# Kernel optimization log

Measured on AMD Instinct MI355X. Metric: run time of the kernel, lower is better.

The kernel has to match this reference:

```python
import jax, jax.numpy as jnp
import numpy as np

DIM = 64
K = 8
B_TAIL = 3.0
HID = 128
BATCH = 131072
MIN_BIN_WIDTH = 1e-3
MIN_BIN_HEIGHT = 1e-3
MIN_DERIVATIVE = 1e-3


def setup_inputs() -> dict:
    key = jax.random.key(0)
    ks = jax.random.split(key, 9)
    nin = DIM // 2
    nout = (3 * K - 1) * (DIM - DIM // 2)
    dims = [nin, HID, HID, HID, nout]
    d = {"x": jax.random.normal(ks[0], (BATCH, DIM), jnp.float32)}
    for i in range(4):
        d[f"W{i+1}"] = jax.random.normal(ks[1 + 2 * i], (dims[i], dims[i + 1]), jnp.float32) / jnp.sqrt(dims[i])
        d[f"b{i+1}"] = jax.random.normal(ks[2 + 2 * i], (dims[i + 1],), jnp.float32) * 0.01
    return d


def _gather(a, idx):
    # a: [..., K or K+1], idx: [...] int -> [...]
    return jnp.take_along_axis(a, idx[..., None], axis=-1)[..., 0]


def _mlp(x, W1, b1, W2, b2, W3, b3, W4, b4):
    h = jax.nn.elu(x @ W1 + b1)
    h = jax.nn.elu(h @ W2 + b2)
    h = jax.nn.elu(h @ W3 + b3)
    return h @ W4 + b4


def _unconstrained_rqs_fwd(inputs, uw, uh, ud, tail_bound):
    # inputs: [B, D2]; uw/uh: [B, D2, K]; ud: [B, D2, K-1]
    num_bins = uw.shape[-1]
    left = bottom = -tail_bound
    right = top = tail_bound

    inside = (inputs >= -tail_bound) & (inputs <= tail_bound)
    x = jnp.clip(inputs, -tail_bound, tail_bound)  # safe values for spline math

    # pad derivatives and pin boundary slopes so spline matches identity tails
    const = float(np.log(np.exp(1.0 - MIN_DERIVATIVE) - 1.0))
    ud = jnp.pad(ud, [(0, 0)] * (ud.ndim - 1) + [(1, 1)], constant_values=const)

    widths = jax.nn.softmax(uw, axis=-1)
    widths = MIN_BIN_WIDTH + (1.0 - MIN_BIN_WIDTH * num_bins) * widths
    cumwidths = jnp.cumsum(widths, axis=-1)
    cumwidths = jnp.pad(cumwidths, [(0, 0)] * (cumwidths.ndim - 1) + [(1, 0)])
    cumwidths = (right - left) * cumwidths + left
    cumwidths = cumwidths.at[..., 0].set(left).at[..., -1].set(right)
    widths = cumwidths[..., 1:] - cumwidths[..., :-1]

    derivatives = MIN_DERIVATIVE + jax.nn.softplus(ud)

    heights = jax.nn.softmax(uh, axis=-1)
    heights = MIN_BIN_HEIGHT + (1.0 - MIN_BIN_HEIGHT * num_bins) * heights
    cumheights = jnp.cumsum(heights, axis=-1)
    cumheights = jnp.pad(cumheights, [(0, 0)] * (cumheights.ndim - 1) + [(1, 0)])
    cumheights = (top - bottom) * cumheights + bottom
    cumheights = cumheights.at[..., 0].set(bottom).at[..., -1].set(top)
    heights = cumheights[..., 1:] - cumheights[..., :-1]

    # searchsorted: number of bin edges <= x, minus one (eps on last edge)
    cw = cumwidths.at[..., -1].add(1e-6)
    bin_idx = jnp.sum((x[..., None] >= cw).astype(jnp.int32), axis=-1) - 1
    bin_idx = jnp.clip(bin_idx, 0, num_bins - 1)

    in_cw = _gather(cumwidths, bin_idx)
    in_w = _gather(widths, bin_idx)
    in_ch = _gather(cumheights, bin_idx)
    in_h = _gather(heights, bin_idx)
    delta = heights / widths
    in_delta = _gather(delta, bin_idx)
    in_d = _gather(derivatives, bin_idx)
    in_d1 = _gather(derivatives[..., 1:], bin_idx)

    theta = (x - in_cw) / in_w
    t1mt = theta * (1.0 - theta)
    numerator = in_h * (in_delta * theta ** 2 + in_d * t1mt)
    denominator = in_delta + (in_d + in_d1 - 2.0 * in_delta) * t1mt
    spline_out = in_ch + numerator / denominator
    deriv_num = in_delta ** 2 * (in_d1 * theta ** 2 + 2.0 * in_delta * t1mt + in_d * (1.0 - theta) ** 2)
    spline_ld = jnp.log(deriv_num) - 2.0 * jnp.log(denominator)

    outputs = jnp.where(inside, spline_out, inputs)
    logabsdet = jnp.where(inside, spline_ld, 0.0)
    return outputs, logabsdet


def reference(x, W1, b1, W2, b2, W3, b3, W4, b4):
    d_half = DIM // 2
    x1, x2 = x[:, :d_half], x[:, d_half:]
    out = _mlp(x1, W1, b1, W2, b2, W3, b3, W4, b4)
    out = out.reshape(-1, DIM - d_half, 3 * K - 1)
    W = out[..., :K]
    H = out[..., K:2 * K]
    D = out[..., 2 * K:]
    y2, ld = _unconstrained_rqs_fwd(x2, W, H, D, B_TAIL)
    log_det = jnp.sum(ld, axis=1)
    return jnp.concatenate([x1, y2], axis=1), log_det
```

## Files before the change

### kernel.cpp

```cpp
#include <hip/hip_runtime.h>
#include <hip/hip_bf16.h>
#include <math.h>

typedef _Float16 f16_t;
typedef _Float16 f16x4 __attribute__((ext_vector_type(4)));
typedef _Float16 f16x8 __attribute__((ext_vector_type(8)));
typedef float f32x4 __attribute__((ext_vector_type(4)));

#define BATCH 131072
#define MTILE 64
#define NBLK (BATCH / MTILE)
#define LOG2E 1.4426950408889634f

#define W1F 0
#define W2F 4096
#define W3F 20480
#define W4F 36864
#define B4S_OFF 67584

__global__ __launch_bounds__(256) void convert_weights_kernel(
    const float* __restrict__ W1, const float* __restrict__ W2,
    const float* __restrict__ W3, const float* __restrict__ W4,
    const float* __restrict__ b4, f16_t* __restrict__ wf,
    float* __restrict__ b4s) {
  int tid = blockIdx.x * 256 + threadIdx.x;
  if (tid >= 16896) {
    int i = tid - 16896;
    if (i < 736) {
      float s = ((i % 23) < 16) ? LOG2E : 1.f;
      b4s[i] = b4[i] * s;
    }
    return;
  }
  int lane = tid & 63;
  int l16 = lane & 15, lhi = lane >> 4;
  const float* W; int ncols, col, k0; bool zero = false; float scale = 1.f;
  if (tid < 512) {
    int n = tid >> 6;
    W = W1; ncols = 128; col = n * 16 + l16; k0 = lhi * 8;
  } else if (tid < 2560) {
    int g = tid - 512; int n = g >> 8, s = (g >> 6) & 3;
    W = W2; ncols = 128; col = n * 16 + l16; k0 = s * 32 + lhi * 8;
  } else if (tid < 4608) {
    int g = tid - 2560; int n = g >> 8, s = (g >> 6) & 3;
    W = W3; ncols = 128; col = n * 16 + l16; k0 = s * 32 + lhi * 8;
  } else {
    int g = tid - 4608; int t = g >> 8, s = (g >> 6) & 3;
    int c = t / 6, n = t - c * 6;
    int colc = n * 16 + l16;
    W = W4; ncols = 736; col = c * 92 + colc; k0 = s * 32 + lhi * 8;
    zero = (colc >= 92);
    if (!zero) scale = ((col % 23) < 16) ? LOG2E : 1.f;
  }
  f16x8 v;
#pragma unroll
  for (int j = 0; j < 8; ++j)
    v[j] = zero ? (f16_t)0.f : (f16_t)(W[(k0 + j) * ncols + col] * scale);
  *(f16x8*)(wf + (size_t)tid * 8) = v;
}

__device__ __forceinline__ float elu(float v) {
  return v > 0.f ? v : (__expf(v) - 1.f);
}

__device__ __forceinline__ void rqs_task(const f16_t* P, float xv,
                                         float& yout, float& ldout) {
  f16x8 pw = *(const f16x8*)P;
  f16x8 ph = *(const f16x8*)(P + 8);
  f16x8 pd = *(const f16x8*)(P + 16);

  float ew[8], sw = 0.f;
#pragma unroll
  for (int i = 0; i < 8; ++i) { ew[i] = exp2f((float)pw[i]); sw += ew[i]; }
  float invw = 0.992f * __builtin_amdgcn_rcpf(sw);
  float cw[8]; cw[0] = -3.f;
  float accw = 0.f;
#pragma unroll
  for (int i = 0; i < 7; ++i) {
    accw += 0.001f + ew[i] * invw;
    cw[i + 1] = -3.f + 6.f * accw;
  }

  float eh[8], sh = 0.f;
#pragma unroll
  for (int i = 0; i < 8; ++i) { eh[i] = exp2f((float)ph[i]); sh += eh[i]; }
  float invh = 0.992f * __builtin_amdgcn_rcpf(sh);
  float ch[8]; ch[0] = -3.f;
  float acch = 0.f;
#pragma unroll
  for (int i = 0; i < 7; ++i) {
    acch += 0.001f + eh[i] * invh;
    ch[i + 1] = -3.f + 6.f * acch;
  }

  float xc = fminf(fmaxf(xv, -3.f), 3.f);
  int bin = 0;
#pragma unroll
  for (int i = 1; i < 8; ++i) bin += (xc >= cw[i]) ? 1 : 0;

  float in_cw = cw[0], in_ch = ch[0];
  float ewsel = ew[0], ehsel = eh[0];
  float sd  = (float)pd[0];
  float sd1 = (float)pd[0];
#pragma unroll
  for (int i = 1; i < 8; ++i) {
    bool g = (bin >= i);
    in_cw = g ? cw[i] : in_cw;  in_ch = g ? ch[i] : in_ch;
    ewsel = g ? ew[i] : ewsel;  ehsel = g ? eh[i] : ehsel;
    sd    = g ? (float)pd[i - 1] : sd;
  }
#pragma unroll
  for (int i = 1; i < 7; ++i)
    sd1 = (bin >= i) ? (float)pd[i] : sd1;

  float in_w = fmaf(ewsel * invw, 6.f, 0.006f);
  float in_h = fmaf(ehsel * invh, 6.f, 0.006f);

  float spd  = fmaxf(sd,  0.f) + __logf(1.f + __expf(-fabsf(sd)));
  float spd1 = fmaxf(sd1, 0.f) + __logf(1.f + __expf(-fabsf(sd1)));
  float in_d  = (bin == 0) ? 1.f : 0.001f + spd;
  float in_d1 = (bin == 7) ? 1.f : 0.001f + spd1;

  float rw = __builtin_amdgcn_rcpf(in_w);
  float dlt = in_h * rw;
  float th = (xc - in_cw) * rw;
  float om = 1.f - th;
  float t1 = th * om;
  float num = in_h * (dlt * th * th + in_d * t1);
  float den = dlt + (in_d + in_d1 - 2.f * dlt) * t1;
  float rden = __builtin_amdgcn_rcpf(den);
  float yo = in_ch + num * rden;
  float dn = dlt * dlt * (in_d1 * th * th + 2.f * dlt * t1 + in_d * om * om);
  float ldv = __logf(dn * rden * rden);
  bool inside = (xv >= -3.f) && (xv <= 3.f);
  yout = inside ? yo : xv;
  ldout = inside ? ldv : 0.f;
}

__device__ __forceinline__ void mid_layer_ip(f16_t* hH,
                                             const f16_t* __restrict__ wseg,
                                             const float* __restrict__ bg,
                                             int wv, int l16, int lhi, int lane) {
  f16x8 a[4];
#pragma unroll
  for (int s = 0; s < 4; ++s)
    a[s] = *(const f16x8*)&hH[(wv * 16 + l16) * 136 + s * 32 + lhi * 8];
#pragma unroll
  for (int n = 0; n < 8; ++n) {
    f32x4 acc = {0.f, 0.f, 0.f, 0.f};
#pragma unroll
    for (int s = 0; s < 4; ++s) {
      f16x8 b = *(const f16x8*)(wseg + (size_t)((n * 4 + s) * 64 + lane) * 8);
      acc = __builtin_amdgcn_mfma_f32_16x16x32_f16(a[s], b, acc, 0, 0, 0);
    }
    float bias = bg[n * 16 + l16];
#pragma unroll
    for (int r = 0; r < 4; ++r)
      hH[(wv * 16 + lhi * 4 + r) * 136 + n * 16 + l16] =
          (f16_t)elu(acc[r] + bias);
  }
}

__global__ __launch_bounds__(256, 3) void nsf_fused_kernel(
    const float* __restrict__ x,
    const float* __restrict__ b1g, const float* __restrict__ b2g,
    const float* __restrict__ b3g, const float* __restrict__ b4s,
    const f16_t* __restrict__ wf,
    float* __restrict__ out) {
  __shared__ f16_t hH[MTILE * 136];
  __shared__ float x2s[MTILE * 33];

  const int tid = threadIdx.x;
  const int lane = tid & 63;
  const int wv = tid >> 6;
  const int l16 = lane & 15, lhi = lane >> 4;
  const int row0 = blockIdx.x * MTILE;

  {
    const float4* x4 = (const float4*)(x + (size_t)row0 * 64);
    float4* o4 = (float4*)(out + (size_t)row0 * 64);
#pragma unroll
    for (int it = 0; it < 4; ++it) {
      int idx = tid + it * 256;
      int row = idx >> 4, q = idx & 15;
      float4 v = x4[row * 16 + q];
      if (q < 8) {
        o4[row * 16 + q] = v;
        f16x4 p = {(f16_t)v.x, (f16_t)v.y, (f16_t)v.z, (f16_t)v.w};
        *(f16x4*)&hH[row * 136 + q * 4] = p;
      } else {
        int cb = row * 33 + (q - 8) * 4;
        x2s[cb + 0] = v.x; x2s[cb + 1] = v.y;
        x2s[cb + 2] = v.z; x2s[cb + 3] = v.w;
      }
    }
  }
  __syncthreads();

  {
    f16x8 a = *(const f16x8*)&hH[(wv * 16 + l16) * 136 + lhi * 8];
#pragma unroll
    for (int n = 0; n < 8; ++n) {
      f16x8 b = *(const f16x8*)(wf + W1F + (size_t)(n * 64 + lane) * 8);
      f32x4 acc = {0.f, 0.f, 0.f, 0.f};
      acc = __builtin_amdgcn_mfma_f32_16x16x32_f16(a, b, acc, 0, 0, 0);
      float bias = b1g[n * 16 + l16];
#pragma unroll
      for (int r = 0; r < 4; ++r)
        hH[(wv * 16 + lhi * 4 + r) * 136 + n * 16 + l16] =
            (f16_t)elu(acc[r] + bias);
    }
  }
  __syncthreads();

  mid_layer_ip(hH, wf + W2F, b2g, wv, l16, lhi, lane);
  __syncthreads();
  mid_layer_ip(hH, wf + W3F, b3g, wv, l16, lhi, lane);
  __syncthreads();

  {
    f16x8 a4[4];
#pragma unroll
    for (int s = 0; s < 4; ++s)
      a4[s] = *(const f16x8*)&hH[(wv * 16 + l16) * 136 + s * 32 + lhi * 8];
    __syncthreads();

    const int srow = tid >> 2;
    const int sjj = tid & 3;
    float ldp = 0.f;

    for (int c = 0; c < 8; ++c) {
#pragma unroll
      for (int n = 0; n < 6; ++n) {
        f32x4 acc = {0.f, 0.f, 0.f, 0.f};
#pragma unroll
        for (int s = 0; s < 4; ++s) {
          f16x8 b = *(const f16x8*)(wf + W4F +
                      (size_t)(((c * 6 + n) * 4 + s) * 64 + lane) * 8);
          acc = __builtin_amdgcn_mfma_f32_16x16x32_f16(a4[s], b, acc, 0, 0, 0);
        }
        int colc = n * 16 + l16;
        if (colc < 92) {
          int dm = (colc * 90) >> 11;
          int j = colc - dm * 23;
          float bias = b4s[c * 92 + colc];
#pragma unroll
          for (int r = 0; r < 4; ++r)
            hH[((wv * 16 + lhi * 4 + r) * 4 + dm) * 24 + j] =
                (f16_t)(acc[r] + bias);
        }
      }
      __builtin_amdgcn_wave_barrier();

      {
        int jg = c * 4 + sjj;
        float xv = x2s[srow * 33 + jg];
        float y0, l0;
        rqs_task(hH + tid * 24, xv, y0, l0);
        out[(size_t)(row0 + srow) * 64 + 32 + jg] = y0;
        ldp += l0;
      }
      __builtin_amdgcn_wave_barrier();
    }

    ldp += __shfl_xor(ldp, 1, 64);
    ldp += __shfl_xor(ldp, 2, 64);
    if ((tid & 3) == 0)
      out[(size_t)BATCH * 64 + row0 + srow] = ldp;
  }
}

extern "C" void kernel_launch(void* const* d_in, const int* in_sizes, int n_in,
                              void* d_out, int out_size, void* d_ws, size_t ws_size,
                              hipStream_t stream) {
  const float* x  = (const float*)d_in[0];
  const float* W1 = (const float*)d_in[1];
  const float* b1 = (const float*)d_in[2];
  const float* W2 = (const float*)d_in[3];
  const float* b2 = (const float*)d_in[4];
  const float* W3 = (const float*)d_in[5];
  const float* b3 = (const float*)d_in[6];
  const float* W4 = (const float*)d_in[7];
  const float* b4 = (const float*)d_in[8];
  f16_t* wf = (f16_t*)d_ws;
  float* b4s = (float*)d_ws + B4S_OFF;
  float* out = (float*)d_out;

  hipLaunchKernelGGL(convert_weights_kernel, dim3(69), dim3(256), 0, stream,
                     W1, W2, W3, W4, b4, wf, b4s);
  hipLaunchKernelGGL(nsf_fused_kernel, dim3(NBLK), dim3(256), 0, stream,
                     x, b1, b2, b3, b4s, wf, out);
}
```

Before: 98.25 us.

## Shrink fused kernel to single-wave 16-row blocks with wave barriers

The fused MLP+spline kernel now uses one 64-thread wavefront per block, each handling 16 rows, instead of four waves handling 64 rows. Block-wide __syncthreads are replaced by wave barriers, because all LDS sharing now happens within one wave. This removes cross-wave synchronisation stalls and lets the scheduler interleave more independent blocks. In exchange the grid grows fourfold, and each block re-reads the full weight set from global memory or cache with no sharing across waves.

```diff
diff --git a/kernel.cpp b/kernel.cpp
--- a/kernel.cpp
+++ b/kernel.cpp
@@ -8,7 +8,7 @@
 typedef float f32x4 __attribute__((ext_vector_type(4)));
 
 #define BATCH 131072
-#define MTILE 64
+#define MTILE 16
 #define NBLK (BATCH / MTILE)
 #define LOG2E 1.4426950408889634f
 
@@ -140,11 +140,11 @@
 __device__ __forceinline__ void mid_layer_ip(f16_t* hH,
                                              const f16_t* __restrict__ wseg,
                                              const float* __restrict__ bg,
-                                             int wv, int l16, int lhi, int lane) {
+                                             int l16, int lhi, int lane) {
   f16x8 a[4];
 #pragma unroll
   for (int s = 0; s < 4; ++s)
-    a[s] = *(const f16x8*)&hH[(wv * 16 + l16) * 136 + s * 32 + lhi * 8];
+    a[s] = *(const f16x8*)&hH[l16 * 136 + s * 32 + lhi * 8];
 #pragma unroll
   for (int n = 0; n < 8; ++n) {
     f32x4 acc = {0.f, 0.f, 0.f, 0.f};
@@ -156,12 +156,11 @@
     float bias = bg[n * 16 + l16];
 #pragma unroll
     for (int r = 0; r < 4; ++r)
-      hH[(wv * 16 + lhi * 4 + r) * 136 + n * 16 + l16] =
-          (f16_t)elu(acc[r] + bias);
-  }
-}
-
-__global__ __launch_bounds__(256, 3) void nsf_fused_kernel(
+      hH[(lhi * 4 + r) * 136 + n * 16 + l16] = (f16_t)elu(acc[r] + bias);
+  }
+}
+
+__global__ __launch_bounds__(64) void nsf_fused_kernel(
     const float* __restrict__ x,
     const float* __restrict__ b1g, const float* __restrict__ b2g,
     const float* __restrict__ b3g, const float* __restrict__ b4s,
@@ -170,9 +169,7 @@
   __shared__ f16_t hH[MTILE * 136];
   __shared__ float x2s[MTILE * 33];
 
-  const int tid = threadIdx.x;
-  const int lane = tid & 63;
-  const int wv = tid >> 6;
+  const int lane = threadIdx.x;
   const int l16 = lane & 15, lhi = lane >> 4;
   const int row0 = blockIdx.x * MTILE;
 
@@ -180,25 +177,25 @@
     const float4* x4 = (const float4*)(x + (size_t)row0 * 64);
     float4* o4 = (float4*)(out + (size_t)row0 * 64);
 #pragma unroll
-    for (int it = 0; it < 4; ++it) {
-      int idx = tid + it * 256;
-      int row = idx >> 4, q = idx & 15;
-      float4 v = x4[row * 16 + q];
-      if (q < 8) {
-        o4[row * 16 + q] = v;
+    for (int i = 0; i < 4; ++i) {
+      int flat = i * 64 + lane;
+      int r = flat >> 4, f = flat & 15;
+      float4 v = x4[r * 16 + f];
+      if (f < 8) {
+        o4[r * 16 + f] = v;
         f16x4 p = {(f16_t)v.x, (f16_t)v.y, (f16_t)v.z, (f16_t)v.w};
-        *(f16x4*)&hH[row * 136 + q * 4] = p;
+        *(f16x4*)&hH[r * 136 + f * 4] = p;
       } else {
-        int cb = row * 33 + (q - 8) * 4;
+        int cb = r * 33 + (f - 8) * 4;
         x2s[cb + 0] = v.x; x2s[cb + 1] = v.y;
         x2s[cb + 2] = v.z; x2s[cb + 3] = v.w;
       }
     }
   }
-  __syncthreads();
+  __builtin_amdgcn_wave_barrier();
 
   {
-    f16x8 a = *(const f16x8*)&hH[(wv * 16 + l16) * 136 + lhi * 8];
+    f16x8 a = *(const f16x8*)&hH[l16 * 136 + lhi * 8];
 #pragma unroll
     for (int n = 0; n < 8; ++n) {
       f16x8 b = *(const f16x8*)(wf + W1F + (size_t)(n * 64 + lane) * 8);
@@ -207,26 +204,25 @@
       float bias = b1g[n * 16 + l16];
 #pragma unroll
       for (int r = 0; r < 4; ++r)
-        hH[(wv * 16 + lhi * 4 + r) * 136 + n * 16 + l16] =
-            (f16_t)elu(acc[r] + bias);
-    }
-  }
-  __syncthreads();
-
-  mid_layer_ip(hH, wf + W2F, b2g, wv, l16, lhi, lane);
-  __syncthreads();
-  mid_layer_ip(hH, wf + W3F, b3g, wv, l16, lhi, lane);
-  __syncthreads();
+        hH[(lhi * 4 + r) * 136 + n * 16 + l16] = (f16_t)elu(acc[r] + bias);
+    }
+  }
+  __builtin_amdgcn_wave_barrier();
+
+  mid_layer_ip(hH, wf + W2F, b2g, l16, lhi, lane);
+  __builtin_amdgcn_wave_barrier();
+  mid_layer_ip(hH, wf + W3F, b3g, l16, lhi, lane);
+  __builtin_amdgcn_wave_barrier();
 
   {
     f16x8 a4[4];
 #pragma unroll
     for (int s = 0; s < 4; ++s)
-      a4[s] = *(const f16x8*)&hH[(wv * 16 + l16) * 136 + s * 32 + lhi * 8];
-    __syncthreads();
-
-    const int srow = tid >> 2;
-    const int sjj = tid & 3;
+      a4[s] = *(const f16x8*)&hH[l16 * 136 + s * 32 + lhi * 8];
+    __builtin_amdgcn_wave_barrier();
+
+    const int srow = lane >> 2;
+    const int sjj = lane & 3;
     float ldp = 0.f;
 
     for (int c = 0; c < 8; ++c) {
@@ -246,8 +242,7 @@
           float bias = b4s[c * 92 + colc];
 #pragma unroll
           for (int r = 0; r < 4; ++r)
-            hH[((wv * 16 + lhi * 4 + r) * 4 + dm) * 24 + j] =
-                (f16_t)(acc[r] + bias);
+            hH[((lhi * 4 + r) * 4 + dm) * 24 + j] = (f16_t)(acc[r] + bias);
         }
       }
       __builtin_amdgcn_wave_barrier();
@@ -256,7 +251,7 @@
         int jg = c * 4 + sjj;
         float xv = x2s[srow * 33 + jg];
         float y0, l0;
-        rqs_task(hH + tid * 24, xv, y0, l0);
+        rqs_task(hH + lane * 24, xv, y0, l0);
         out[(size_t)(row0 + srow) * 64 + 32 + jg] = y0;
         ldp += l0;
       }
@@ -265,7 +260,7 @@
 
     ldp += __shfl_xor(ldp, 1, 64);
     ldp += __shfl_xor(ldp, 2, 64);
-    if ((tid & 3) == 0)
+    if ((lane & 3) == 0)
       out[(size_t)BATCH * 64 + row0 + srow] = ldp;
   }
 }
@@ -288,6 +283,6 @@
 
   hipLaunchKernelGGL(convert_weights_kernel, dim3(69), dim3(256), 0, stream,
                      W1, W2, W3, W4, b4, wf, b4s);
-  hipLaunchKernelGGL(nsf_fused_kernel, dim3(NBLK), dim3(256), 0, stream,
+  hipLaunchKernelGGL(nsf_fused_kernel, dim3(NBLK), dim3(64), 0, stream,
                      x, b1, b2, b3, b4s, wf, out);
 }
```

After: 101.3 us. +3.1%, slower.
